# Kernel tuning notes

Hardware: AMD Instinct MI355X
Metric: run time of the kernel (lower is better)

Reference implementation:

```python
import jax, jax.numpy as jnp
import numpy as np

# MORRConfig_20um_MQ ring parameters
A = 0.8578   # attenuation factor a
R = 0.8985   # coupling factor r

IN_C, OUT_C, KS, STRIDE, PAD, MB = 32, 64, 3, 1, 1, 8
WIN = IN_C * KS * KS                      # 288 = kernel_size^2 * in_channel
WIN_PAD = ((WIN + MB - 1) // MB) * MB     # padded to multiple of miniblock
OUT_PAD = ((OUT_C + MB - 1) // MB) * MB
Q = WIN_PAD // MB                         # grid_dim_x = 36
P = OUT_PAD // MB                         # grid_dim_y = 8
MORR_GAIN = (100.0 / (WIN // MB)) ** 0.5  # input power normalization


def mrr_tr(phi):
    # all-pass MORR roundtrip-phase -> transmission intensity
    # T = (a^2 - 2ar cos(phi) + r^2) / (1 - 2ar cos(phi) + (ar)^2)
    c = 2.0 * A * R * jnp.cos(phi)
    return (A * A + R * R - c) / (1.0 + (A * R) ** 2 - c)


def im2col(x):
    # torch F.unfold ordering: feature dim ordered (C, ki, kj)
    B, C, H, W = x.shape
    xp = jnp.pad(x, ((0, 0), (0, 0), (PAD, PAD), (PAD, PAD)))
    Ho = (H + 2 * PAD - KS) // STRIDE + 1
    Wo = (W + 2 * PAD - KS) // STRIDE + 1
    cols = [xp[:, :, i:i + Ho * STRIDE:STRIDE, j:j + Wo * STRIDE:STRIDE]
            for i in range(KS) for j in range(KS)]
    p = jnp.stack(cols, axis=2)               # [B, C, KS*KS, Ho, Wo]
    return p.reshape(B, C * KS * KS, Ho * Wo), Ho, Wo


def setup_inputs() -> dict:
    key = jax.random.key(0)
    k1, k2, k3 = jax.random.split(key, 3)
    x = jax.random.uniform(k1, (8, IN_C, 64, 64), dtype=jnp.float32)  # intensity-encoded, nonneg
    weight = jax.random.uniform(k2, (P, Q, MB), dtype=jnp.float32) * 0.2  # nonneg MORR weights
    morr_output_scale = jax.random.normal(k3, (max(1, Q // 2) + 1,), dtype=jnp.float32) * 0.1
    return {"x": x, "weight": weight, "morr_output_scale": morr_output_scale}


def reference(x, weight, morr_output_scale):
    B = x.shape[0]
    cols, Ho, Wo = im2col(x)
    xb = cols.transpose(0, 2, 1)
    if WIN_PAD > WIN:
        xb = jnp.pad(xb, ((0, 0), (0, 0), (0, WIN_PAD - WIN)))
    xb = xb.reshape(-1, Q, MB)                # [Bs, Q, MB]
    inten = (xb * xb) * MORR_GAIN             # optical intensity (power-normalized)

    # block-circulant weighted phase accumulation == circular conv per (p,q) block, via rFFT
    Wf = jnp.fft.rfft(weight, axis=-1)        # [P, Q, MBf]
    Xf = jnp.fft.rfft(inten, axis=-1)         # [Bs, Q, MBf]
    phase = jnp.fft.irfft(Xf[:, None, :, :] * Wf[None], n=MB, axis=-1)  # [Bs, P, Q, MB]

    tr = mrr_tr(phase)                        # MORR nonlinear transfer

    # differential rails: learnable balancing factor per block-column pair (+1 pad scale)
    half = morr_output_scale[:-1]             # [Q//2]
    if Q % 2 == 0:
        scale = jnp.concatenate([half, -half])                              # [Q]
    else:
        scale = jnp.concatenate([half, morr_output_scale[-1:], -half])      # [Q]

    out = jnp.einsum("bpqk,q->bpk", tr, scale).reshape(-1, OUT_PAD)[:, :OUT_C]
    out = out.reshape(B, Ho * Wo, OUT_C).transpose(0, 2, 1).reshape(B, OUT_C, Ho, Wo)
    return out
```

## Files before the change

kernel.cpp:

```cpp
#include <hip/hip_runtime.h>

#define IN_C 32
#define HW 64
#define Q_N 36

typedef float f32x4 __attribute__((ext_vector_type(4)));
typedef short s16x8 __attribute__((ext_vector_type(8)));
typedef short s16x4 __attribute__((ext_vector_type(4)));

#define WEXP_OFF 0
#define ZW_OFF   73728
#define SCL_OFF  74240
#define GX2_OFF  75776

__device__ __forceinline__ unsigned short f2bf(float f) {
    union { float f; unsigned int u; } v; v.f = f;
    unsigned int t = v.u + 0x7FFFu + ((v.u >> 16) & 1u);
    return (unsigned short)(t >> 16);
}

#define A_C 0.8578f
#define R_C 0.8985f
#define S_C (A_C*A_C + R_C*R_C)
#define D_C (1.f + (A_C*R_C)*(A_C*R_C))
#define C2_C (2.f*A_C*R_C)
#define E_C (S_C - D_C)
#define GI_C (1.6666666666666667f * 0.15915494309189535f)

__global__ __launch_bounds__(512)
void morr_pre(const float* __restrict__ x,
              const float* __restrict__ weight,
              const float* __restrict__ mos,
              unsigned char* __restrict__ ws)
{
    const int tid = threadIdx.x;
    const int blk = blockIdx.x;
    if (blk < 512) {
        const int i = (blk * 512 + tid) * 4;
        float4 v = *(const float4*)(x + i);
        unsigned short o0 = f2bf(GI_C * v.x * v.x);
        unsigned short o1 = f2bf(GI_C * v.y * v.y);
        unsigned short o2 = f2bf(GI_C * v.z * v.z);
        unsigned short o3 = f2bf(GI_C * v.w * v.w);
        s16x4 o = {(short)o0, (short)o1, (short)o2, (short)o3};
        *(s16x4*)(ws + GX2_OFF + (size_t)i * 2) = o;
    } else {
        unsigned short* wexp = (unsigned short*)(ws + WEXP_OFF);
#pragma unroll
        for (int it = 0; it < 72; ++it) {
            const int idx = tid + 512 * it;
            const int q  = idx >> 9;
            const int mt = (idx >> 7) & 3;
            const int pr = (idx >> 3) & 15;
            const int j  = idx & 7;
            const int pk = mt * 16 + pr;
            const int p  = pk >> 3, k = pk & 7;
            wexp[idx] = f2bf(weight[p * 288 + q * 8 + ((k - j) & 7)]);
        }
        if (tid < 128) ((float*)(ws + ZW_OFF))[tid] = 0.f;
        if (tid < Q_N)
            ((float*)(ws + SCL_OFF))[tid] =
                ((tid < 18) ? mos[tid] : -mos[tid - 18]) * E_C;
    }
}

__global__ __launch_bounds__(512, 4)
void morr_conv_kernel(const unsigned char* __restrict__ ws,
                      float* __restrict__ out)
{
    __shared__ __align__(16) unsigned short Aim[64 * 296];

    const int tid = threadIdx.x;
    const int blk = blockIdx.x;
    const int b   = blk >> 6;
    const int row = blk & 63;

    const unsigned short* gx2 = (const unsigned short*)(ws + GX2_OFF);

    {
        const int px = tid & 63;
        const int g  = tid >> 6;
        unsigned short buf[36];
#pragma unroll
        for (int cc = 0; cc < 4; ++cc) {
            const int c = g * 4 + cc;
            const unsigned short* xc = gx2 + ((b * IN_C + c) << 12);
#pragma unroll
            for (int ki = 0; ki < 3; ++ki) {
                const int gh = row + ki - 1;
                const bool rok = (unsigned)gh < 64u;
#pragma unroll
                for (int kj = 0; kj < 3; ++kj) {
                    const int gw = px + kj - 1;
                    unsigned short v = 0;
                    if (rok && (unsigned)gw < 64u) v = xc[(gh << 6) + gw];
                    buf[cc * 9 + ki * 3 + kj] = v;
                }
            }
        }
        unsigned short* dst = Aim + px * 296 + g * 36;
#pragma unroll
        for (int i = 0; i < 9; ++i) {
            s16x4 v = {(short)buf[i*4], (short)buf[i*4+1],
                       (short)buf[i*4+2], (short)buf[i*4+3]};
            *(s16x4*)(dst + i * 4) = v;
        }
    }
    __syncthreads();

    const int wv = tid >> 6;
    const int l  = tid & 63;
    const int ll = l & 15;
    const int lh = l >> 4;
    const int nt = wv & 3;
    const int m0 = (wv >> 2) * 2;

    const unsigned short* bB = Aim + (nt * 16 + ll) * 296;
    const unsigned short* aW;
    int qs;
    if (l < 16) { aW = (const unsigned short*)(ws + WEXP_OFF) + (m0 * 16 + ll) * 8; qs = 512; }
    else        { aW = (const unsigned short*)(ws + ZW_OFF);                        qs = 0;   }
    const float* __restrict__ sp = (const float*)(ws + SCL_OFF);

    float acc[8];
#pragma unroll
    for (int i = 0; i < 8; ++i) acc[i] = 0.f;

    const f32x4 cz = {0.f, 0.f, 0.f, 0.f};

#pragma unroll
    for (int q = 0; q < Q_N; ++q) {
        s16x8 bfrag = *(const s16x8*)(bB + q * 8);
        s16x8 a0 = *(const s16x8*)(aW + q * qs);
        s16x8 a1 = *(const s16x8*)(aW + q * qs + 128);
        f32x4 d0 = __builtin_amdgcn_mfma_f32_16x16x32_bf16(a0, bfrag, cz, 0, 0, 0);
        f32x4 d1 = __builtin_amdgcn_mfma_f32_16x16x32_bf16(a1, bfrag, cz, 0, 0, 0);
        const float sc = sp[q];
#pragma unroll
        for (int r = 0; r < 4; ++r) {
            float c0 = __builtin_amdgcn_cosf(d0[r]);
            acc[r]     = fmaf(sc, __builtin_amdgcn_rcpf(fmaf(-C2_C, c0, D_C)), acc[r]);
            float c1 = __builtin_amdgcn_cosf(d1[r]);
            acc[4 + r] = fmaf(sc, __builtin_amdgcn_rcpf(fmaf(-C2_C, c1, D_C)), acc[4 + r]);
        }
    }

    const int col = nt * 16 + ll;
#pragma unroll
    for (int t = 0; t < 2; ++t) {
#pragma unroll
        for (int r = 0; r < 4; ++r) {
            const int pk = (m0 + t) * 16 + lh * 4 + r;
            out[(b * 64 + pk) * (HW * HW) + row * HW + col] = acc[t * 4 + r];
        }
    }
}

extern "C" void kernel_launch(void* const* d_in, const int* in_sizes, int n_in,
                              void* d_out, int out_size, void* d_ws, size_t ws_size,
                              hipStream_t stream) {
    const float* x      = (const float*)d_in[0];
    const float* weight = (const float*)d_in[1];
    const float* mos    = (const float*)d_in[2];
    float* out = (float*)d_out;
    unsigned char* ws = (unsigned char*)d_ws;

    hipLaunchKernelGGL(morr_pre, dim3(513), dim3(512), 0, stream, x, weight, mos, ws);
    hipLaunchKernelGGL(morr_conv_kernel, dim3(512), dim3(512), 0, stream, ws, out);
}
```

Baseline: 83.50 us.

## Split conv blocks into 16-pixel row segments with 256 threads each

```diff
diff --git a/kernel.cpp b/kernel.cpp
--- a/kernel.cpp
+++ b/kernel.cpp
@@ -38,11 +38,8 @@
     if (blk < 512) {
         const int i = (blk * 512 + tid) * 4;
         float4 v = *(const float4*)(x + i);
-        unsigned short o0 = f2bf(GI_C * v.x * v.x);
-        unsigned short o1 = f2bf(GI_C * v.y * v.y);
-        unsigned short o2 = f2bf(GI_C * v.z * v.z);
-        unsigned short o3 = f2bf(GI_C * v.w * v.w);
-        s16x4 o = {(short)o0, (short)o1, (short)o2, (short)o3};
+        s16x4 o = {(short)f2bf(GI_C * v.x * v.x), (short)f2bf(GI_C * v.y * v.y),
+                   (short)f2bf(GI_C * v.z * v.z), (short)f2bf(GI_C * v.w * v.w)};
         *(s16x4*)(ws + GX2_OFF + (size_t)i * 2) = o;
     } else {
         unsigned short* wexp = (unsigned short*)(ws + WEXP_OFF);
@@ -64,47 +61,52 @@
     }
 }
 
-__global__ __launch_bounds__(512, 4)
+__global__ __launch_bounds__(256, 8)
 void morr_conv_kernel(const unsigned char* __restrict__ ws,
                       float* __restrict__ out)
 {
-    __shared__ __align__(16) unsigned short Aim[64 * 296];
+    __shared__ __align__(16) unsigned short Aim[16 * 296];
 
     const int tid = threadIdx.x;
     const int blk = blockIdx.x;
-    const int b   = blk >> 6;
-    const int row = blk & 63;
+    const int b   = blk >> 8;
+    const int rem = blk & 255;
+    const int row = rem >> 2;
+    const int w0  = (rem & 3) << 4;
 
     const unsigned short* gx2 = (const unsigned short*)(ws + GX2_OFF);
 
     {
-        const int px = tid & 63;
-        const int g  = tid >> 6;
-        unsigned short buf[36];
+        const int px = tid & 15;
+        const int g  = tid >> 4;
+        unsigned int wbuf[9];
 #pragma unroll
-        for (int cc = 0; cc < 4; ++cc) {
-            const int c = g * 4 + cc;
+        for (int cc = 0; cc < 2; ++cc) {
+            const int c = 2 * g + cc;
             const unsigned short* xc = gx2 + ((b * IN_C + c) << 12);
+            unsigned short e[9];
 #pragma unroll
             for (int ki = 0; ki < 3; ++ki) {
                 const int gh = row + ki - 1;
                 const bool rok = (unsigned)gh < 64u;
 #pragma unroll
                 for (int kj = 0; kj < 3; ++kj) {
-                    const int gw = px + kj - 1;
+                    const int gw = w0 + px + kj - 1;
                     unsigned short v = 0;
                     if (rok && (unsigned)gw < 64u) v = xc[(gh << 6) + gw];
-                    buf[cc * 9 + ki * 3 + kj] = v;
+                    e[ki * 3 + kj] = v;
                 }
             }
+#pragma unroll
+            for (int i = 0; i < 4; ++i)
+                wbuf[cc * 4 + i + cc] = (unsigned)e[2*i + (cc ? 1 : 0)] |
+                                        ((unsigned)e[2*i + 1 + (cc ? 1 : 0)] << 16);
+            if (cc == 0) wbuf[4] = (unsigned)e[8];
+            else         wbuf[4] |= ((unsigned)e[0] << 16);
         }
-        unsigned short* dst = Aim + px * 296 + g * 36;
+        unsigned int* dst = (unsigned int*)((unsigned char*)Aim + px * 592 + g * 36);
 #pragma unroll
-        for (int i = 0; i < 9; ++i) {
-            s16x4 v = {(short)buf[i*4], (short)buf[i*4+1],
-                       (short)buf[i*4+2], (short)buf[i*4+3]};
-            *(s16x4*)(dst + i * 4) = v;
-        }
+        for (int i = 0; i < 9; ++i) dst[i] = wbuf[i];
     }
     __syncthreads();
 
@@ -112,47 +114,35 @@
     const int l  = tid & 63;
     const int ll = l & 15;
     const int lh = l >> 4;
-    const int nt = wv & 3;
-    const int m0 = (wv >> 2) * 2;
 
-    const unsigned short* bB = Aim + (nt * 16 + ll) * 296;
+    const unsigned short* bB = Aim + ll * 296;
     const unsigned short* aW;
     int qs;
-    if (l < 16) { aW = (const unsigned short*)(ws + WEXP_OFF) + (m0 * 16 + ll) * 8; qs = 512; }
+    if (l < 16) { aW = (const unsigned short*)(ws + WEXP_OFF) + (wv * 16 + ll) * 8; qs = 512; }
     else        { aW = (const unsigned short*)(ws + ZW_OFF);                        qs = 0;   }
     const float* __restrict__ sp = (const float*)(ws + SCL_OFF);
 
-    float acc[8];
-#pragma unroll
-    for (int i = 0; i < 8; ++i) acc[i] = 0.f;
-
+    float acc[4] = {0.f, 0.f, 0.f, 0.f};
     const f32x4 cz = {0.f, 0.f, 0.f, 0.f};
 
 #pragma unroll
     for (int q = 0; q < Q_N; ++q) {
         s16x8 bfrag = *(const s16x8*)(bB + q * 8);
-        s16x8 a0 = *(const s16x8*)(aW + q * qs);
-        s16x8 a1 = *(const s16x8*)(aW + q * qs + 128);
-        f32x4 d0 = __builtin_amdgcn_mfma_f32_16x16x32_bf16(a0, bfrag, cz, 0, 0, 0);
-        f32x4 d1 = __builtin_amdgcn_mfma_f32_16x16x32_bf16(a1, bfrag, cz, 0, 0, 0);
+        s16x8 a = *(const s16x8*)(aW + q * qs);
+        f32x4 d = __builtin_amdgcn_mfma_f32_16x16x32_bf16(a, bfrag, cz, 0, 0, 0);
         const float sc = sp[q];
 #pragma unroll
         for (int r = 0; r < 4; ++r) {
-            float c0 = __builtin_amdgcn_cosf(d0[r]);
-            acc[r]     = fmaf(sc, __builtin_amdgcn_rcpf(fmaf(-C2_C, c0, D_C)), acc[r]);
-            float c1 = __builtin_amdgcn_cosf(d1[r]);
-            acc[4 + r] = fmaf(sc, __builtin_amdgcn_rcpf(fmaf(-C2_C, c1, D_C)), acc[4 + r]);
+            float c0 = __builtin_amdgcn_cosf(d[r]);
+            acc[r] = fmaf(sc, __builtin_amdgcn_rcpf(fmaf(-C2_C, c0, D_C)), acc[r]);
         }
     }
 
-    const int col = nt * 16 + ll;
+    const int col = w0 + ll;
 #pragma unroll
-    for (int t = 0; t < 2; ++t) {
-#pragma unroll
-        for (int r = 0; r < 4; ++r) {
-            const int pk = (m0 + t) * 16 + lh * 4 + r;
-            out[(b * 64 + pk) * (HW * HW) + row * HW + col] = acc[t * 4 + r];
-        }
+    for (int r = 0; r < 4; ++r) {
+        const int pk = wv * 16 + lh * 4 + r;
+        out[(b * 64 + pk) * (HW * HW) + row * HW + col] = acc[r];
     }
 }
 
@@ -166,5 +156,5 @@
     unsigned char* ws = (unsigned char*)d_ws;
 
     hipLaunchKernelGGL(morr_pre, dim3(513), dim3(512), 0, stream, x, weight, mos, ws);
-    hipLaunchKernelGGL(morr_conv_kernel, dim3(512), dim3(512), 0, stream, ws, out);
+    hipLaunchKernelGGL(morr_conv_kernel, dim3(2048), dim3(256), 0, stream, ws, out);
 }
```

Result: slower. 87.50 us (+4.8%).
